# Performance work log

Hardware: AMD Instinct MI355X
Metric: run time of the kernel (lower is better)

The kernel has to match this reference:

```python
import jax, jax.numpy as jnp
import numpy as np

B, N, IN_DIM, OUT_DIM, H = 4, 2048, 256, 256, 8
ATN = OUT_DIM // H  # 32


def setup_inputs() -> dict:
    key = jax.random.key(0)
    k1, k2, k3, k4, k5 = jax.random.split(key, 5)
    x = jax.random.normal(k1, (B, N, IN_DIM), dtype=jnp.float32)
    adj = jax.random.uniform(k2, (B, N, N), dtype=jnp.float32)
    # stacked per-head Linear weights/biases and bilinear corelation matrices
    W = jax.random.normal(k3, (H, IN_DIM, ATN), dtype=jnp.float32) / np.sqrt(IN_DIM)
    b = jax.random.normal(k4, (H, ATN), dtype=jnp.float32) * 0.01
    C = jax.random.normal(k5, (H, ATN, ATN), dtype=jnp.float32) / np.sqrt(ATN)
    return {"x": x, "adj": adj, "W": W, "b": b, "C": C}


def reference(x, adj, W, b, C):
    # x: [B,N,in_dim]; adj: [B,N,N]; W: [H,in_dim,atn]; b: [H,atn]; C: [H,atn,atn]
    # per-head linear projection -> [B,H,N,atn]
    xt = jnp.einsum('bni,hio->bhno', x, W) + b[None, :, None, :]
    # bilinear scores: (xt @ C^T) @ xt^T ; torch einsum 'akj,ij->aki' contracts
    # the second index of corelation, i.e. xC = xt @ C.T
    xC = jnp.einsum('bhno,hpo->bhnp', xt, C)          # [B,H,N,atn]
    scores = jnp.einsum('bhnp,bhmp->bhnm', xC, xt)    # [B,H,N,N]
    alpha = jnp.tanh(scores * adj[:, None, :, :])     # mask then tanh
    heads = jnp.einsum('bhnm,bhmo->bhno', alpha, xt)  # [B,H,N,atn]
    # concat heads on feature dim -> [B,N,H*atn]
    out = jnp.transpose(heads, (0, 2, 1, 3)).reshape(x.shape[0], x.shape[1], -1)
    return out
```

## Files before the change

kernel.cpp:

```cpp
#include <hip/hip_runtime.h>
#include <hip/hip_bf16.h>


typedef __bf16 bf16;
typedef __attribute__((ext_vector_type(8))) __bf16 bf16x8;
typedef __attribute__((ext_vector_type(4))) __bf16 bf16x4;
typedef __attribute__((ext_vector_type(4))) float  f32x4;

#define MFMA(a, b, c) __builtin_amdgcn_mfma_f32_16x16x32_bf16(a, b, c, 0, 0, 0)

#define GLDS16(g, l) __builtin_amdgcn_global_load_lds(                        \
        (const __attribute__((address_space(1))) void*)(g),                   \
        (__attribute__((address_space(3))) void*)(l), 16, 0, 0)

#define WAITVM6() __builtin_amdgcn_s_waitcnt(0x0F76)
#define WAITVM5() __builtin_amdgcn_s_waitcnt(0x0F75)
#define WAITVM0() __builtin_amdgcn_s_waitcnt(0x0F70)
#define FENCE()   __builtin_amdgcn_sched_barrier(0)
#define BAR()     __builtin_amdgcn_s_barrier()

__device__ __forceinline__ float fast_tanh(float x) {
    float t   = x * x;
    float num = x * __builtin_fmaf(t, t + 105.0f, 945.0f);
    float den = __builtin_fmaf(t, __builtin_fmaf(t, 15.0f, 420.0f), 945.0f);
    float r   = num * __builtin_amdgcn_rcpf(den);
    return __builtin_amdgcn_fmed3f(r, -1.0f, 1.0f);
}

#define BB   4
#define NN   2048
#define IND  256
#define HH   8
#define ATN  32

#define OFF_XBF   0u
#define OFF_XT    4194304u
#define OFF_XC    8388608u
#define OFF_XTT   12582912u
#define OFF_WT    16777216u
#define OFF_CB    16908288u
#define OFF_SLAB  16924672u

__global__ __launch_bounds__(256) void k_prep(const float* __restrict__ x,
                                              const float* __restrict__ W,
                                              const float* __restrict__ C,
                                              bf16* __restrict__ xbf,
                                              bf16* __restrict__ WT,
                                              bf16* __restrict__ Cb) {
    int tid = blockIdx.x * 256 + threadIdx.x;
    if (tid < 524288) {
        float4 v = ((const float4*)x)[tid];
        bf16x4 o;
        o[0] = (bf16)v.x; o[1] = (bf16)v.y; o[2] = (bf16)v.z; o[3] = (bf16)v.w;
        *(bf16x4*)(xbf + (size_t)tid * 4) = o;
    } else if (tid < 524288 + 65536) {
        int t = tid - 524288;
        int h = t >> 13, r = t & 8191, i = r >> 5, o = r & 31;
        WT[(h * 32 + o) * 256 + i] = (bf16)W[t];
    } else if (tid < 524288 + 65536 + 8192) {
        int t = tid - (524288 + 65536);
        Cb[t] = (bf16)C[t];
    }
}

__global__ __launch_bounds__(256) void k_proj(const bf16* __restrict__ xbf,
                                              const bf16* __restrict__ WT,
                                              const bf16* __restrict__ Cb,
                                              const float* __restrict__ bias,
                                              bf16* __restrict__ xt,
                                              bf16* __restrict__ xc,
                                              bf16* __restrict__ xtT) {
    __shared__ bf16 ldsA_all[4][32 * 40];
    __shared__ bf16 ldsB_all[4][32 * 40];
    int bid = blockIdx.x;
    int ntg = bid & 15, h = (bid >> 4) & 7, b = bid >> 7;
    int wave = threadIdx.x >> 6;
    int lane = threadIdx.x & 63;
    int nt = ntg * 4 + wave;
    int n0 = nt * 32;
    int c = lane & 15, q = lane >> 4;
    bf16* ldsA = ldsA_all[wave];
    bf16* ldsB = ldsB_all[wave];

    f32x4 acc[2][2] = {};
    const bf16* xrow0 = xbf + ((size_t)(b * NN + n0 + c) * IND + q * 8);
    const bf16* xrow1 = xbf + ((size_t)(b * NN + n0 + 16 + c) * IND + q * 8);
    const bf16* wrow0 = WT + ((h * 32 + c) * IND + q * 8);
    const bf16* wrow1 = WT + ((h * 32 + 16 + c) * IND + q * 8);
#pragma unroll
    for (int k0 = 0; k0 < IND; k0 += 32) {
        bf16x8 a0 = *(const bf16x8*)(xrow0 + k0);
        bf16x8 a1 = *(const bf16x8*)(xrow1 + k0);
        bf16x8 w0 = *(const bf16x8*)(wrow0 + k0);
        bf16x8 w1 = *(const bf16x8*)(wrow1 + k0);
        acc[0][0] = MFMA(a0, w0, acc[0][0]);
        acc[0][1] = MFMA(a0, w1, acc[0][1]);
        acc[1][0] = MFMA(a1, w0, acc[1][0]);
        acc[1][1] = MFMA(a1, w1, acc[1][1]);
    }
    float bv[2] = { bias[h * 32 + c], bias[h * 32 + 16 + c] };
    size_t bh = (size_t)(b * HH + h);
#pragma unroll
    for (int nq = 0; nq < 2; ++nq)
#pragma unroll
        for (int oq = 0; oq < 2; ++oq)
#pragma unroll
            for (int r = 0; r < 4; ++r)
                ldsA[(nq * 16 + q * 4 + r) * 40 + oq * 16 + c] =
                    (bf16)(acc[nq][oq][r] + bv[oq]);
    f32x4 acc2[2][2] = {};
    bf16x8 aL0 = *(const bf16x8*)(ldsA + (c) * 40 + q * 8);
    bf16x8 aL1 = *(const bf16x8*)(ldsA + (16 + c) * 40 + q * 8);
    bf16x8 c0 = *(const bf16x8*)(Cb + h * 1024 + (c) * 32 + q * 8);
    bf16x8 c1 = *(const bf16x8*)(Cb + h * 1024 + (16 + c) * 32 + q * 8);
    acc2[0][0] = MFMA(aL0, c0, acc2[0][0]);
    acc2[0][1] = MFMA(aL0, c1, acc2[0][1]);
    acc2[1][0] = MFMA(aL1, c0, acc2[1][0]);
    acc2[1][1] = MFMA(aL1, c1, acc2[1][1]);
#pragma unroll
    for (int nq = 0; nq < 2; ++nq)
#pragma unroll
        for (int pq = 0; pq < 2; ++pq)
#pragma unroll
            for (int r = 0; r < 4; ++r)
                ldsB[(nq * 16 + q * 4 + r) * 40 + pq * 16 + c] =
                    (bf16)acc2[nq][pq][r];

    {
        int n = lane >> 1, half = lane & 1;
        bf16x8 t0 = *(const bf16x8*)(ldsA + n * 40 + half * 16);
        bf16x8 t1 = *(const bf16x8*)(ldsA + n * 40 + half * 16 + 8);
        bf16* dst = xt + (bh * NN + n0 + n) * ATN + half * 16;
        *(bf16x8*)(dst) = t0;
        *(bf16x8*)(dst + 8) = t1;
        bf16x8 u0 = *(const bf16x8*)(ldsB + n * 40 + half * 16);
        bf16x8 u1 = *(const bf16x8*)(ldsB + n * 40 + half * 16 + 8);
        bf16* dst2 = xc + (bh * NN + n0 + n) * ATN + half * 16;
        *(bf16x8*)(dst2) = u0;
        *(bf16x8*)(dst2 + 8) = u1;
    }
    {
        int o = lane >> 1, nh = lane & 1;
        bf16x8 t0, t1;
#pragma unroll
        for (int i = 0; i < 8; ++i) {
            t0[i] = ldsA[(nh * 16 + i) * 40 + o];
            t1[i] = ldsA[(nh * 16 + 8 + i) * 40 + o];
        }
        bf16* dst = xtT + (bh * ATN + o) * NN + n0 + nh * 16;
        *(bf16x8*)(dst) = t0;
        *(bf16x8*)(dst + 8) = t1;
    }
}

__global__ __launch_bounds__(512, 4) void k_attn(const float* __restrict__ adj,
                                                 const bf16* __restrict__ xt,
                                                 const bf16* __restrict__ xc,
                                                 const bf16* __restrict__ xtT,
                                                 bf16* __restrict__ sl0,
                                                 bf16* __restrict__ sl1,
                                                 bf16* __restrict__ sl2,
                                                 float* __restrict__ out) {
    __shared__ float adjlds[4 * 1024];
    int bid = blockIdx.x;
    int chunk = bid >> 8;
    int bn = bid & 255;
    int nt = bn & 63, b = bn >> 6;
    int n0 = nt * 32;
    int wave = threadIdx.x >> 6;
    int lane = threadIdx.x & 63;
    int c = lane & 15, q = lane >> 4;
    int p = 8 * (c >> 2) + (c & 3);
    size_t bh = (size_t)(b * HH + wave);
    const bf16* xt_h = xt + bh * NN * ATN;
    const bf16* xc_h = xc + bh * NN * ATN;
    const bf16* xtT_h = xtT + bh * ATN * NN;
    const float* adj_b = adj + (size_t)b * NN * NN;
    const int m_beg = chunk * 512;

    int nloc = wave * 8 + (lane >> 3);
    int gsub = (lane & 7) ^ (lane >> 3);
    const float* gA = adj_b + (size_t)(n0 + nloc) * NN + gsub * 4 + m_beg;

#define DMA(t) do { if (wave < 4)                                              \
        GLDS16(gA + (t) * 32, adjlds + ((t) & 3) * 1024 + wave * 256);         \
    } while (0)

    bf16x8 bXC0 = *(const bf16x8*)(xc_h + (n0 + c) * ATN + q * 8);
    bf16x8 bXC1 = *(const bf16x8*)(xc_h + (n0 + 16 + c) * ATN + q * 8);
    f32x4 accO[2][2] = {};
    const f32x4 z = {0.f, 0.f, 0.f, 0.f};

    bf16x8 xA0e, xA1e, oA0e, oA1e, xA0o, xA1o, oA0o, oA1o;
#define REGS_E(t) do { int m0 = m_beg + (t) * 32;                              \
        xA0e = *(const bf16x8*)(xt_h + (size_t)(m0 + p) * ATN + q * 8);        \
        xA1e = *(const bf16x8*)(xt_h + (size_t)(m0 + p + 4) * ATN + q * 8);    \
        oA0e = *(const bf16x8*)(xtT_h + (size_t)(c) * NN + m0 + q * 8);        \
        oA1e = *(const bf16x8*)(xtT_h + (size_t)(16 + c) * NN + m0 + q * 8);   \
    } while (0)
#define REGS_O(t) do { int m0 = m_beg + (t) * 32;                              \
        xA0o = *(const bf16x8*)(xt_h + (size_t)(m0 + p) * ATN + q * 8);        \
        xA1o = *(const bf16x8*)(xt_h + (size_t)(m0 + p + 4) * ATN + q * 8);    \
        oA0o = *(const bf16x8*)(xtT_h + (size_t)(c) * NN + m0 + q * 8);        \
        oA1o = *(const bf16x8*)(xtT_h + (size_t)(16 + c) * NN + m0 + q * 8);   \
    } while (0)

    int ad00 = c * 32 + ((2 * q) ^ (c & 7)) * 4;
    int ad01 = c * 32 + ((2 * q + 1) ^ (c & 7)) * 4;
    int ad10 = (16 + c) * 32 + ((2 * q) ^ (c & 7)) * 4;
    int ad11 = (16 + c) * 32 + ((2 * q + 1) ^ (c & 7)) * 4;

#define COMPUTE(t, xA0, xA1, oA0, oA1) do {                                    \
        const float* lb = adjlds + ((t) & 3) * 1024;                           \
        f32x4 A00 = *(const f32x4*)(lb + ad00);                                \
        f32x4 A01 = *(const f32x4*)(lb + ad01);                                \
        f32x4 A10 = *(const f32x4*)(lb + ad10);                                \
        f32x4 A11 = *(const f32x4*)(lb + ad11);                                \
        f32x4 S0a = MFMA(xA0, bXC0, z);             \
        f32x4 S0b = MFMA(xA1, bXC0, z);             \
        f32x4 S1a = MFMA(xA0, bXC1, z);             \
        f32x4 S1b = MFMA(xA1, bXC1, z);                                        \
        bf16x8 P0, P1;                                                         \
        _Pragma("unroll") for (int r = 0; r < 4; ++r) {                        \
            P0[r]     = (bf16)fast_tanh(S0a[r] * A00[r]);                      \
            P0[4 + r] = (bf16)fast_tanh(S0b[r] * A01[r]);                      \
            P1[r]     = (bf16)fast_tanh(S1a[r] * A10[r]);                      \
            P1[4 + r] = (bf16)fast_tanh(S1b[r] * A11[r]);                      \
        }                                                                      \
        accO[0][0] = MFMA(oA0, P0, accO[0][0]);                                \
        accO[0][1] = MFMA(oA0, P1, accO[0][1]);                                \
        accO[1][0] = MFMA(oA1, P0, accO[1][0]);                                \
        accO[1][1] = MFMA(oA1, P1, accO[1][1]);                                \
    } while (0)

    REGS_E(0);
    DMA(0);
    DMA(1);
    for (int tt = 0; tt < 14; tt += 2) {
        DMA(tt + 2);
        REGS_O(tt + 1);
        FENCE(); WAITVM6(); BAR(); FENCE();
        COMPUTE(tt, xA0e, xA1e, oA0e, oA1e);
        DMA(tt + 3);
        REGS_E(tt + 2);
        FENCE(); WAITVM6(); BAR(); FENCE();
        COMPUTE(tt + 1, xA0o, xA1o, oA0o, oA1o);
    }
    REGS_O(15);
    FENCE(); WAITVM5(); BAR(); FENCE();
    COMPUTE(14, xA0e, xA1e, oA0e, oA1e);
    FENCE(); WAITVM0(); BAR(); FENCE();
    COMPUTE(15, xA0o, xA1o, oA0o, oA1o);

#undef DMA
#undef REGS_E
#undef REGS_O
#undef COMPUTE

    if (chunk == 3) {
#pragma unroll
        for (int oq = 0; oq < 2; ++oq)
#pragma unroll
            for (int nq = 0; nq < 2; ++nq) {
                size_t n = n0 + nq * 16 + c;
                *(f32x4*)&out[((size_t)b * NN + n) * 256 + wave * 32 + oq * 16 + 4 * q] =
                    accO[oq][nq];
            }
    } else {
        bf16* sl = (chunk == 0) ? sl0 : (chunk == 1 ? sl1 : sl2);
#pragma unroll
        for (int oq = 0; oq < 2; ++oq)
#pragma unroll
            for (int nq = 0; nq < 2; ++nq) {
                size_t n = n0 + nq * 16 + c;
                bf16x4 v;
#pragma unroll
                for (int r = 0; r < 4; ++r) v[r] = (bf16)accO[oq][nq][r];
                *(bf16x4*)&sl[((size_t)b * NN + n) * 256 + wave * 32 + oq * 16 + 4 * q] = v;
            }
    }
}

__global__ __launch_bounds__(256) void k_reduce(const bf16* __restrict__ sl0,
                                                const bf16* __restrict__ sl1,
                                                const bf16* __restrict__ sl2,
                                                float* __restrict__ out) {
    int i = blockIdx.x * 256 + threadIdx.x;
    f32x4 a = ((const f32x4*)out)[i];
    bf16x4 s0 = ((const bf16x4*)sl0)[i];
    bf16x4 s1 = ((const bf16x4*)sl1)[i];
    bf16x4 s2 = ((const bf16x4*)sl2)[i];
#pragma unroll
    for (int r = 0; r < 4; ++r)
        a[r] += (float)s0[r] + (float)s1[r] + (float)s2[r];
    ((f32x4*)out)[i] = a;
}

extern "C" void kernel_launch(void* const* d_in, const int* in_sizes, int n_in,
                              void* d_out, int out_size, void* d_ws, size_t ws_size,
                              hipStream_t stream) {
    const float* x    = (const float*)d_in[0];
    const float* adj  = (const float*)d_in[1];
    const float* W    = (const float*)d_in[2];
    const float* bias = (const float*)d_in[3];
    const float* C    = (const float*)d_in[4];
    float* out = (float*)d_out;

    char* ws = (char*)d_ws;
    bf16*  xbf  = (bf16*)(ws + OFF_XBF);
    bf16*  xt   = (bf16*)(ws + OFF_XT);
    bf16*  xc   = (bf16*)(ws + OFF_XC);
    bf16*  xtT  = (bf16*)(ws + OFF_XTT);
    bf16*  WT   = (bf16*)(ws + OFF_WT);
    bf16*  Cb   = (bf16*)(ws + OFF_CB);
    bf16*  sl0  = (bf16*)(ws + OFF_XBF);
    bf16*  sl1  = (bf16*)(ws + OFF_SLAB);
    bf16*  sl2  = (bf16*)(ws + OFF_SLAB + 4194304u);

    k_prep<<<2336, 256, 0, stream>>>(x, W, C, xbf, WT, Cb);
    k_proj<<<512, 256, 0, stream>>>(xbf, WT, Cb, bias, xt, xc, xtT);
    k_attn<<<1024, 512, 0, stream>>>(adj, xt, xc, xtT, sl0, sl1, sl2, out);
    k_reduce<<<2048, 256, 0, stream>>>(sl0, sl1, sl2, out);
}
```

Before: 176.2 us.

## Deepen adj LDS ring to six stages and use exp-based tanh

The adjacency DMA ring in LDS grows from four to six slots. The loop is restructured to process two tiles per barrier with prefetch depth four, which halves the number of barriers and issues register loads for the next pair after compute. The rational tanh approximation is replaced by an exp2/rcp formulation, which has fewer ALU ops but different accuracy and may overflow for large inputs. The larger LDS footprint and the extra live registers could reduce occupancy.

```diff
diff --git a/kernel.cpp b/kernel.cpp
--- a/kernel.cpp
+++ b/kernel.cpp
@@ -13,18 +13,15 @@
         (const __attribute__((address_space(1))) void*)(g),                   \
         (__attribute__((address_space(3))) void*)(l), 16, 0, 0)
 
-#define WAITVM6() __builtin_amdgcn_s_waitcnt(0x0F76)
-#define WAITVM5() __builtin_amdgcn_s_waitcnt(0x0F75)
-#define WAITVM0() __builtin_amdgcn_s_waitcnt(0x0F70)
-#define FENCE()   __builtin_amdgcn_sched_barrier(0)
-#define BAR()     __builtin_amdgcn_s_barrier()
+#define WAITVM10() __builtin_amdgcn_s_waitcnt(0x0F7A)
+#define WAITVM8()  __builtin_amdgcn_s_waitcnt(0x0F78)
+#define FENCE()    __builtin_amdgcn_sched_barrier(0)
+#define BAR()      __builtin_amdgcn_s_barrier()
 
 __device__ __forceinline__ float fast_tanh(float x) {
-    float t   = x * x;
-    float num = x * __builtin_fmaf(t, t + 105.0f, 945.0f);
-    float den = __builtin_fmaf(t, __builtin_fmaf(t, 15.0f, 420.0f), 945.0f);
-    float r   = num * __builtin_amdgcn_rcpf(den);
-    return __builtin_amdgcn_fmed3f(r, -1.0f, 1.0f);
+    float e = __builtin_amdgcn_exp2f(x * 2.88539008177792681f);
+    float r = __builtin_amdgcn_rcpf(e + 1.0f);
+    return __builtin_fmaf(-2.0f, r, 1.0f);
 }
 
 #define BB   4
@@ -161,7 +158,7 @@
                                                  bf16* __restrict__ sl1,
                                                  bf16* __restrict__ sl2,
                                                  float* __restrict__ out) {
-    __shared__ float adjlds[4 * 1024];
+    __shared__ float adjlds[6 * 1024];
     int bid = blockIdx.x;
     int chunk = bid >> 8;
     int bn = bid & 255;
@@ -183,7 +180,7 @@
     const float* gA = adj_b + (size_t)(n0 + nloc) * NN + gsub * 4 + m_beg;
 
 #define DMA(t) do { if (wave < 4)                                              \
-        GLDS16(gA + (t) * 32, adjlds + ((t) & 3) * 1024 + wave * 256);         \
+        GLDS16(gA + (t) * 32, adjlds + ((t) % 6) * 1024 + wave * 256);         \
     } while (0)
 
     bf16x8 bXC0 = *(const bf16x8*)(xc_h + (n0 + c) * ATN + q * 8);
@@ -211,7 +208,7 @@
     int ad11 = (16 + c) * 32 + ((2 * q + 1) ^ (c & 7)) * 4;
 
 #define COMPUTE(t, xA0, xA1, oA0, oA1) do {                                    \
-        const float* lb = adjlds + ((t) & 3) * 1024;                           \
+        const float* lb = adjlds + ((t) % 6) * 1024;                           \
         f32x4 A00 = *(const f32x4*)(lb + ad00);                                \
         f32x4 A01 = *(const f32x4*)(lb + ad01);                                \
         f32x4 A10 = *(const f32x4*)(lb + ad10);                                \
@@ -233,23 +230,19 @@
         accO[1][1] = MFMA(oA1, P1, accO[1][1]);                                \
     } while (0)
 
-    REGS_E(0);
-    DMA(0);
-    DMA(1);
-    for (int tt = 0; tt < 14; tt += 2) {
-        DMA(tt + 2);
-        REGS_O(tt + 1);
-        FENCE(); WAITVM6(); BAR(); FENCE();
-        COMPUTE(tt, xA0e, xA1e, oA0e, oA1e);
-        DMA(tt + 3);
-        REGS_E(tt + 2);
-        FENCE(); WAITVM6(); BAR(); FENCE();
+    DMA(0); DMA(1); DMA(2); DMA(3);
+    REGS_E(0); REGS_O(1);
+#pragma unroll
+    for (int tt = 0; tt <= 12; tt += 2) {
+        FENCE(); WAITVM10(); BAR(); FENCE();
+        if (tt + 4 < 16) { DMA(tt + 4); DMA(tt + 5); }
+        COMPUTE(tt,     xA0e, xA1e, oA0e, oA1e);
         COMPUTE(tt + 1, xA0o, xA1o, oA0o, oA1o);
-    }
-    REGS_O(15);
-    FENCE(); WAITVM5(); BAR(); FENCE();
+        FENCE();
+        REGS_E(tt + 2); REGS_O(tt + 3);
+    }
+    FENCE(); WAITVM8(); BAR(); FENCE();
     COMPUTE(14, xA0e, xA1e, oA0e, oA1e);
-    FENCE(); WAITVM0(); BAR(); FENCE();
     COMPUTE(15, xA0o, xA1o, oA0o, oA1o);
 
 #undef DMA
```

New measurement: 168.7 us. 1.04x faster.
